# Kernel tuning notes

Measured on AMD Instinct MI355X. Metric: run time of the kernel, lower is better.

The kernel has to match this reference:

```python
import jax, jax.numpy as jnp
import numpy as np

D_MODEL = 1024
N_BLOCKS = 4
D_STATE = 16
D_CONV = 4
EXPAND = 2
DT_RANK = 64  # ceil(1024/16)
D_INNER = EXPAND * D_MODEL
BATCH = 2
SEQLEN = 1024


def setup_inputs() -> dict:
    key = jax.random.key(0)
    ks = jax.random.split(key, 8)
    s = 0.02
    f = lambda k, sh: (jax.random.normal(k, sh, dtype=jnp.float32) * s)
    return {
        "x": jax.random.normal(ks[0], (BATCH, SEQLEN, D_MODEL), dtype=jnp.float32),
        "norm_w": jnp.ones((N_BLOCKS, D_MODEL), jnp.float32),
        "norm_b": jnp.zeros((N_BLOCKS, D_MODEL), jnp.float32),
        "in_proj_w": f(ks[1], (N_BLOCKS, D_MODEL, 2 * D_INNER)),
        "conv_w": f(ks[2], (N_BLOCKS, D_INNER, D_CONV)),
        "conv_b": jnp.zeros((N_BLOCKS, D_INNER), jnp.float32),
        "xproj_w": f(ks[3], (N_BLOCKS, D_INNER, DT_RANK + 2 * D_STATE)),
        "dtproj_w": f(ks[4], (N_BLOCKS, DT_RANK, D_INNER)),
        "dtproj_b": jnp.full((N_BLOCKS, D_INNER), -4.6, jnp.float32),  # softplus ~ 0.01
        "A_log": jnp.tile(jnp.log(jnp.arange(1, D_STATE + 1, dtype=jnp.float32))[None, None, :], (N_BLOCKS, D_INNER, 1)),
        "skip_D": jnp.ones((N_BLOCKS, D_INNER), jnp.float32),
        "out_proj_w": f(ks[5], (N_BLOCKS, D_INNER, D_MODEL)),
        "fn_w": jnp.ones((D_MODEL,), jnp.float32),
        "fn_b": jnp.zeros((D_MODEL,), jnp.float32),
    }


def _layer_norm(x, w, b):
    m = jnp.mean(x, -1, keepdims=True)
    v = jnp.mean((x - m) ** 2, -1, keepdims=True)
    return (x - m) * jax.lax.rsqrt(v + 1e-5) * w + b


def _selective_scan(u, dt, A, Bm, Cm, Dp):
    # u, dt: (B,L,E)  A: (E,N)  Bm, Cm: (B,L,N)  Dp: (E,)
    dA = jnp.exp(dt[..., None] * A)                 # (B,L,E,N) ZOH discretization of A
    dBu = (dt * u)[..., None] * Bm[:, :, None, :]   # (B,L,E,N) Euler discretization of B*u

    def step(h, inp):
        dA_t, dBu_t, C_t = inp
        h = dA_t * h + dBu_t                        # (B,E,N)
        y = jnp.einsum('ben,bn->be', h, C_t)
        return h, y

    h0 = jnp.zeros((u.shape[0], u.shape[2], A.shape[1]), u.dtype)
    xs = (jnp.moveaxis(dA, 1, 0), jnp.moveaxis(dBu, 1, 0), jnp.moveaxis(Cm, 1, 0))
    _, ys = jax.lax.scan(step, h0, xs)
    y = jnp.moveaxis(ys, 0, 1)                      # (B,L,E)
    return y + u * Dp


def _mamba(x, in_w, cw, cb, xw, dtw, dtb, A_log, Dp, ow):
    L = x.shape[1]
    xz = x @ in_w                                   # (B,L,2E)
    u, z = jnp.split(xz, 2, axis=-1)
    K = cw.shape[1]
    up = jnp.pad(u, ((0, 0), (K - 1, 0), (0, 0)))   # causal depthwise conv
    conv = cb + sum(up[:, k:k + L, :] * cw[:, k] for k in range(K))
    u = jax.nn.silu(conv)
    dbl = u @ xw                                    # (B,L,R+2N)
    dt = jax.nn.softplus(dbl[..., :DT_RANK] @ dtw + dtb)
    Bm = dbl[..., DT_RANK:DT_RANK + D_STATE]
    Cm = dbl[..., DT_RANK + D_STATE:]
    A = -jnp.exp(A_log)
    y = _selective_scan(u, dt, A, Bm, Cm, Dp)
    y = y * jax.nn.silu(z)                          # gating branch
    return y @ ow


def _forward(x, norm_w, norm_b, in_proj_w, conv_w, conv_b, xproj_w, dtproj_w, dtproj_b, A_log, skip_D, out_proj_w, fn_w, fn_b):
    for i in range(N_BLOCKS):
        h = _layer_norm(x, norm_w[i], norm_b[i])
        h = _mamba(h, in_proj_w[i], conv_w[i], conv_b[i], xproj_w[i], dtproj_w[i], dtproj_b[i], A_log[i], skip_D[i], out_proj_w[i])
        x = x + h                                   # pre-norm residual
    return _layer_norm(x, fn_w, fn_b)


def reference(x, norm_w, norm_b, in_proj_w, conv_w, conv_b, xproj_w, dtproj_w, dtproj_b, A_log, skip_D, out_proj_w, fn_w, fn_b):
    return _forward(x, norm_w, norm_b, in_proj_w, conv_w, conv_b, xproj_w, dtproj_w, dtproj_b, A_log, skip_D, out_proj_w, fn_w, fn_b)
```

## Files before the change

kernel.cpp:

```cpp
#include <hip/hip_runtime.h>
#include <hip/hip_bf16.h>
#include <math.h>

#define BATCH 2
#define SEQLEN 1024
#define DMODEL 1024
#define DINNER 2048
#define DSTATE 16
#define DTRANK 64
#define XDIM 96
#define KCONV 4
#define NBLOCKS 4
#define MROWS (BATCH*SEQLEN)

#define NCHUNK 32
#define CLEN (SEQLEN/NCHUNK)
#define SUN 4

typedef short bf16x8 __attribute__((ext_vector_type(8)));
typedef unsigned short u16x8 __attribute__((ext_vector_type(8)));
typedef float f32x4 __attribute__((ext_vector_type(4)));

__device__ __forceinline__ unsigned short f2bf(float x) {
    union { float f; unsigned u; } c; c.f = x;
    unsigned r = c.u + 0x7FFFu + ((c.u >> 16) & 1u);
    return (unsigned short)(r >> 16);
}
__device__ __forceinline__ float bf2f(unsigned short h) {
    union { unsigned u; float f; } c; c.u = (unsigned)h << 16;
    return c.f;
}

__device__ __forceinline__ void gload16(const void* src, void* dst) {
    __builtin_amdgcn_global_load_lds(
        (const __attribute__((address_space(1))) void*)src,
        (__attribute__((address_space(3))) void*)dst, 16, 0, 0);
}

__global__ __launch_bounds__(256) void lnc_k(const float* __restrict__ x,
    const float* __restrict__ w, const float* __restrict__ b,
    float* __restrict__ resid, unsigned short* __restrict__ out)
{
    int row = blockIdx.x;
    int tid = threadIdx.x;
    size_t off = (size_t)row * DMODEL + tid * 4;
    float4 v = *(const float4*)(x + off);
    *(float4*)(resid + off) = v;
    float s  = v.x + v.y + v.z + v.w;
    float sq = v.x*v.x + v.y*v.y + v.z*v.z + v.w*v.w;
    #pragma unroll
    for (int o = 32; o > 0; o >>= 1) {
        s  += __shfl_down(s, o);
        sq += __shfl_down(sq, o);
    }
    __shared__ float ss[4], sq4[4];
    int wid = tid >> 6;
    if ((tid & 63) == 0) { ss[wid] = s; sq4[wid] = sq; }
    __syncthreads();
    if (tid == 0) {
        ss[0]  = ss[0] + ss[1] + ss[2] + ss[3];
        sq4[0] = sq4[0] + sq4[1] + sq4[2] + sq4[3];
    }
    __syncthreads();
    float mean = ss[0] * (1.0f / DMODEL);
    float var  = sq4[0] * (1.0f / DMODEL) - mean * mean;
    float rstd = rsqrtf(var + 1e-5f);
    float4 wv = *(const float4*)(w + tid * 4);
    float4 bv = *(const float4*)(b + tid * 4);
    ushort4 h;
    h.x = f2bf((v.x - mean) * rstd * wv.x + bv.x);
    h.y = f2bf((v.y - mean) * rstd * wv.y + bv.y);
    h.z = f2bf((v.z - mean) * rstd * wv.z + bv.z);
    h.w = f2bf((v.w - mean) * rstd * wv.w + bv.w);
    *(ushort4*)(out + off) = h;
}

template<int FINAL>
__global__ __launch_bounds__(256) void predln_k(
    const float* __restrict__ pout, float* __restrict__ resid,
    const float* __restrict__ w, const float* __restrict__ b,
    unsigned short* __restrict__ hb16, float* __restrict__ fout)
{
    int row = blockIdx.x;
    int tid = threadIdx.x;
    const size_t MN = (size_t)MROWS * DMODEL;
    size_t off = (size_t)row * DMODEL + tid * 4;
    float4 p0 = *(const float4*)(pout + off);
    float4 p1 = *(const float4*)(pout + off + MN);
    float4 p2 = *(const float4*)(pout + off + 2 * MN);
    float4 p3 = *(const float4*)(pout + off + 3 * MN);
    float4 r  = *(const float4*)(resid + off);
    float4 v;
    v.x = r.x + (p0.x + p1.x) + (p2.x + p3.x);
    v.y = r.y + (p0.y + p1.y) + (p2.y + p3.y);
    v.z = r.z + (p0.z + p1.z) + (p2.z + p3.z);
    v.w = r.w + (p0.w + p1.w) + (p2.w + p3.w);
    if (!FINAL) *(float4*)(resid + off) = v;

    float s  = v.x + v.y + v.z + v.w;
    float sq = v.x*v.x + v.y*v.y + v.z*v.z + v.w*v.w;
    #pragma unroll
    for (int o = 32; o > 0; o >>= 1) {
        s  += __shfl_down(s, o);
        sq += __shfl_down(sq, o);
    }
    __shared__ float ss[4], sq4[4];
    int wid = tid >> 6;
    if ((tid & 63) == 0) { ss[wid] = s; sq4[wid] = sq; }
    __syncthreads();
    if (tid == 0) {
        ss[0]  = ss[0] + ss[1] + ss[2] + ss[3];
        sq4[0] = sq4[0] + sq4[1] + sq4[2] + sq4[3];
    }
    __syncthreads();
    float mean = ss[0] * (1.0f / DMODEL);
    float var  = sq4[0] * (1.0f / DMODEL) - mean * mean;
    float rstd = rsqrtf(var + 1e-5f);
    float4 wv = *(const float4*)(w + tid * 4);
    float4 bv = *(const float4*)(b + tid * 4);
    float o0 = (v.x - mean) * rstd * wv.x + bv.x;
    float o1 = (v.y - mean) * rstd * wv.y + bv.y;
    float o2 = (v.z - mean) * rstd * wv.z + bv.z;
    float o3 = (v.w - mean) * rstd * wv.w + bv.w;
    if (FINAL) {
        *(float4*)(fout + off) = make_float4(o0, o1, o2, o3);
    } else {
        ushort4 h;
        h.x = f2bf(o0); h.y = f2bf(o1); h.z = f2bf(o2); h.w = f2bf(o3);
        *(ushort4*)(hb16 + off) = h;
    }
}

__global__ __launch_bounds__(256) void wtr2_k(
    const float* __restrict__ W, unsigned short* __restrict__ WT,
    int N, int K, long long wstride, long long wtstride)
{
    const float* Wl = W + (size_t)blockIdx.z * wstride;
    unsigned short* WTl = WT + (size_t)blockIdx.z * wtstride;
    __shared__ float T[64][65];
    int n0 = blockIdx.x * 64, k0 = blockIdx.y * 64;
    int tid = threadIdx.x;
    int kk = tid >> 4, nn = (tid & 15) * 4;
    #pragma unroll
    for (int p = 0; p < 4; ++p) {
        float4 v = make_float4(0.f, 0.f, 0.f, 0.f);
        if (n0 + nn + 4 <= N)
            v = *(const float4*)(Wl + (size_t)(k0 + p * 16 + kk) * N + n0 + nn);
        T[p * 16 + kk][nn + 0] = v.x;
        T[p * 16 + kk][nn + 1] = v.y;
        T[p * 16 + kk][nn + 2] = v.z;
        T[p * 16 + kk][nn + 3] = v.w;
    }
    __syncthreads();
    int n2 = tid >> 4, k2 = (tid & 15) * 4;
    #pragma unroll
    for (int p = 0; p < 4; ++p) {
        int nrow = n0 + p * 16 + n2;
        ushort4 h = {0, 0, 0, 0};
        if (nrow < N) {
            h.x = f2bf(T[k2 + 0][p * 16 + n2]);
            h.y = f2bf(T[k2 + 1][p * 16 + n2]);
            h.z = f2bf(T[k2 + 2][p * 16 + n2]);
            h.w = f2bf(T[k2 + 3][p * 16 + n2]);
        }
        *(ushort4*)(WTl + (size_t)nrow * K + k0 + k2) = h;
    }
}

template<int EPI, int BN, int SWZX = 0, int SWZY = 0>
__global__ __launch_bounds__(256) void mgemm6_k(
    const unsigned short* __restrict__ A,
    const unsigned short* __restrict__ BT,
    float* __restrict__ out0, float* __restrict__ out1,
    const float* __restrict__ bias,
    int N, int Kf, int Kloc)
{
    constexpr int WN = BN / 2;
    constexpr int NJ = WN / 16;
    __shared__ unsigned short As[3][128 * 32];
    __shared__ unsigned short Bs[3][BN * 32];
    int tid = threadIdx.x;
    int lane = tid & 63, w = tid >> 6;
    int wr = w >> 1, wc = w & 1;
    int bxx = blockIdx.x, byy = blockIdx.y;
    if constexpr (SWZX > 0) {
        constexpr int TOT = SWZX * SWZY;
        int f = bxx + SWZX * byy;
        int nf = (f & 7) * (TOT / 8) + (f >> 3);
        bxx = nf % SWZX; byy = nf / SWZX;
    }
    int m0 = byy * 128, n0 = bxx * BN;
    int lr = lane & 15, G = lane >> 4;

    int ra0 = w * 32 + (lane >> 2);
    int ra1 = ra0 + 16;
    int ga0 = (lane & 3) ^ ((ra0 >> 1) & 3);
    int ga1 = (lane & 3) ^ ((ra1 >> 1) & 3);
    int rb0 = w * (BN / 4) + (lane >> 2);
    int gb0 = (lane & 3) ^ ((rb0 >> 1) & 3);
    int rb1 = rb0 + 16;
    int gb1 = (lane & 3) ^ ((rb1 >> 1) & 3);

    int kz = blockIdx.z * Kloc;
    const unsigned short* pa0 = A  + (size_t)(m0 + ra0) * Kf + kz + ga0 * 8;
    const unsigned short* pa1 = A  + (size_t)(m0 + ra1) * Kf + kz + ga1 * 8;
    const unsigned short* pb0 = BT + (size_t)(n0 + rb0) * Kf + kz + gb0 * 8;
    const unsigned short* pb1 = BT + (size_t)(n0 + rb1) * Kf + kz + gb1 * 8;
    int dA0 = (w * 32) * 32, dA1 = dA0 + 16 * 32;
    int dB0 = (w * (BN / 4)) * 32, dB1 = dB0 + 16 * 32;

#define ISSUE(tt, bufi) do {                                   \
        gload16(pa0 + (tt) * 32, &As[bufi][dA0]);              \
        gload16(pa1 + (tt) * 32, &As[bufi][dA1]);              \
        gload16(pb0 + (tt) * 32, &Bs[bufi][dB0]);              \
        if (BN == 128) gload16(pb1 + (tt) * 32, &Bs[bufi][dB1]); \
    } while (0)

    f32x4 acc[4][NJ] = {};
    int T = Kloc / 32;

    ISSUE(0, 0);
    if (T > 1) ISSUE(1, 1);

    int cur = 0;
    for (int t = 0; t < T; ++t) {
        if (t + 1 < T) {
            if constexpr (BN == 128)
                asm volatile("s_waitcnt vmcnt(4)" ::: "memory");
            else
                asm volatile("s_waitcnt vmcnt(3)" ::: "memory");
        } else {
            asm volatile("s_waitcnt vmcnt(0)" ::: "memory");
        }
        __builtin_amdgcn_s_barrier();
        if (t + 2 < T) {
            int nb = cur + 2; if (nb >= 3) nb -= 3;
            ISSUE(t + 2, nb);
        }
        bf16x8 af[4], bfr[NJ];
        #pragma unroll
        for (int i = 0; i < 4; ++i) {
            int r = wr * 64 + i * 16 + lr;
            af[i] = *(const bf16x8*)&As[cur][r * 32 + ((G ^ ((r >> 1) & 3)) << 3)];
        }
        #pragma unroll
        for (int j = 0; j < NJ; ++j) {
            int r = wc * WN + j * 16 + lr;
            bfr[j] = *(const bf16x8*)&Bs[cur][r * 32 + ((G ^ ((r >> 1) & 3)) << 3)];
        }
        #pragma unroll
        for (int i = 0; i < 4; ++i)
            #pragma unroll
            for (int j = 0; j < NJ; ++j)
                acc[i][j] = __builtin_amdgcn_mfma_f32_16x16x32_bf16(
                    af[i], bfr[j], acc[i][j], 0, 0, 0);
        __builtin_amdgcn_s_barrier();
        cur = (cur + 1 == 3) ? 0 : cur + 1;
    }
#undef ISSUE

    int rbase = m0 + wr * 64 + (lane >> 4) * 4;
    int cbase = n0 + wc * WN + lr;
    #pragma unroll
    for (int i = 0; i < 4; ++i)
        #pragma unroll
        for (int j = 0; j < NJ; ++j)
            #pragma unroll
            for (int r = 0; r < 4; ++r) {
                int row = rbase + i * 16 + r;
                int col = cbase + j * 16;
                float c = acc[i][j][r];
                if (EPI == 0) {
                    if (col < DINNER)
                        ((unsigned short*)out0)[(size_t)row * DINNER + col] = f2bf(c);
                    else
                        ((unsigned short*)out1)[(size_t)row * DINNER + (col - DINNER)] = f2bf(c);
                } else if (EPI == 2) {
                    out0[(size_t)blockIdx.z * MROWS * N + (size_t)row * N + col] = c;
                } else if (EPI == 3) {
                    if (col < XDIM)
                        out0[(size_t)blockIdx.z * MROWS * XDIM +
                             (size_t)row * XDIM + col] = c;
                } else {
                    float cc = c + bias[col];
                    cc = fmaxf(cc, 0.f) + log1pf(__expf(-fabsf(cc)));
                    ((unsigned short*)out0)[(size_t)row * N + col] = f2bf(cc);
                }
            }
}

#define XSPLIT 16
__global__ __launch_bounds__(256) void xprojR_k(
    const float* __restrict__ part, float* __restrict__ dbl,
    unsigned short* __restrict__ db64)
{
    int idx = blockIdx.x * 256 + threadIdx.x;
    float s = 0.f;
    #pragma unroll
    for (int k = 0; k < XSPLIT; ++k)
        s += part[(size_t)k * MROWS * XDIM + idx];
    dbl[idx] = s;
    int col = idx % XDIM;
    if (col < DTRANK)
        db64[(size_t)(idx / XDIM) * DTRANK + col] = f2bf(s);
}

__global__ __launch_bounds__(256) void conv_k(const unsigned short* __restrict__ u,
    const float* __restrict__ cw, const float* __restrict__ cb,
    unsigned short* __restrict__ out)
{
    int idx = blockIdx.x * 256 + threadIdx.x;
    int c8 = idx & (DINNER / 8 - 1);
    int t  = (idx >> 8) & (SEQLEN - 1);
    int b  = idx >> 18;
    int e0 = c8 * 8;
    size_t base = (size_t)b * SEQLEN * DINNER + (size_t)t * DINNER + e0;
    u16x8 rows[KCONV];
    #pragma unroll
    for (int k = 0; k < KCONV; ++k) {
        int tt = t + k - (KCONV - 1);
        u16x8 zv = {0,0,0,0,0,0,0,0};
        rows[k] = (tt >= 0) ?
            *(const u16x8*)(u + base + (size_t)(k - (KCONV - 1)) * DINNER) : zv;
    }
    u16x8 o;
    #pragma unroll
    for (int j = 0; j < 8; ++j) {
        float4 wv = *(const float4*)(cw + (size_t)(e0 + j) * KCONV);
        float acc = cb[e0 + j];
        acc = fmaf(bf2f(rows[0][j]), wv.x, acc);
        acc = fmaf(bf2f(rows[1][j]), wv.y, acc);
        acc = fmaf(bf2f(rows[2][j]), wv.z, acc);
        acc = fmaf(bf2f(rows[3][j]), wv.w, acc);
        o[j] = f2bf(acc / (1.f + __expf(-acc)));
    }
    *(u16x8*)(out + base) = o;
}

template<int CTRL>
__device__ __forceinline__ float qadd(float x) {
    int y = __builtin_amdgcn_update_dpp(0, __float_as_int(x), CTRL, 0xF, 0xF, true);
    return x + __int_as_float(y);
}

__global__ __launch_bounds__(512) void scan_k(
    const unsigned short* __restrict__ dt, const unsigned short* __restrict__ uc,
    const float* __restrict__ dbl, const unsigned short* __restrict__ z,
    const float* __restrict__ A_log, const float* __restrict__ Dp,
    unsigned short* __restrict__ yout)
{
    __shared__ float sAlo[NCHUNK][8][2][4], sAhi[NCHUNK][8][2][4];
    __shared__ float sBlo[NCHUNK][8][2][4], sBhi[NCHUNK][8][2][4];
    int tid = threadIdx.x;
    int sub = tid & 1;
    int ei  = (tid >> 1) & 7;
    int ch  = tid >> 4;
    int bid = blockIdx.x;
    int blk = (bid & 7) * 64 + (bid >> 3);
    int eg  = blk & 255;
    int b   = blk >> 8;
    int e   = eg * 8 + ei;

    const float L2E = 1.4426950408889634f;
    float AstL2[8];
    {
        const float* ap = A_log + (size_t)e * DSTATE + sub * 8;
        #pragma unroll
        for (int q = 0; q < 2; ++q) {
            float4 v = *(const float4*)(ap + q * 4);
            AstL2[q * 4 + 0] = -__expf(v.x) * L2E;
            AstL2[q * 4 + 1] = -__expf(v.y) * L2E;
            AstL2[q * 4 + 2] = -__expf(v.z) * L2E;
            AstL2[q * 4 + 3] = -__expf(v.w) * L2E;
        }
    }
    size_t base_e = (size_t)b * SEQLEN * DINNER + e;
    size_t base_x = (size_t)b * SEQLEN * XDIM + DTRANK + sub * 8;
    int t0c = ch * CLEN;

    float h[8] = {0.f, 0.f, 0.f, 0.f, 0.f, 0.f, 0.f, 0.f};
    float ssum = 0.f;
    for (int t0 = t0c; t0 < t0c + CLEN; t0 += SUN) {
        float sdt[SUN], su[SUN];
        #pragma unroll
        for (int u = 0; u < SUN; ++u) {
            size_t te = base_e + (size_t)(t0 + u) * DINNER;
            sdt[u] = bf2f(dt[te]);
            su[u]  = bf2f(uc[te]);
        }
        #pragma unroll
        for (int u = 0; u < SUN; ++u) {
            const float* dx = dbl + base_x + (size_t)(t0 + u) * XDIM;
            float4 bn0 = *(const float4*)(dx);
            float4 bn1 = *(const float4*)(dx + 4);
            float dtu = sdt[u] * su[u];
            ssum += sdt[u];
            h[0] = fmaf(__builtin_amdgcn_exp2f(sdt[u] * AstL2[0]), h[0], dtu * bn0.x);
            h[1] = fmaf(__builtin_amdgcn_exp2f(sdt[u] * AstL2[1]), h[1], dtu * bn0.y);
            h[2] = fmaf(__builtin_amdgcn_exp2f(sdt[u] * AstL2[2]), h[2], dtu * bn0.z);
            h[3] = fmaf(__builtin_amdgcn_exp2f(sdt[u] * AstL2[3]), h[3], dtu * bn0.w);
            h[4] = fmaf(__builtin_amdgcn_exp2f(sdt[u] * AstL2[4]), h[4], dtu * bn1.x);
            h[5] = fmaf(__builtin_amdgcn_exp2f(sdt[u] * AstL2[5]), h[5], dtu * bn1.y);
            h[6] = fmaf(__builtin_amdgcn_exp2f(sdt[u] * AstL2[6]), h[6], dtu * bn1.z);
            h[7] = fmaf(__builtin_amdgcn_exp2f(sdt[u] * AstL2[7]), h[7], dtu * bn1.w);
        }
    }
    float a_[8];
    #pragma unroll
    for (int i = 0; i < 8; ++i) a_[i] = __builtin_amdgcn_exp2f(AstL2[i] * ssum);
    *(f32x4*)&sAlo[ch][ei][sub][0] = *(f32x4*)&a_[0];
    *(f32x4*)&sAhi[ch][ei][sub][0] = *(f32x4*)&a_[4];
    *(f32x4*)&sBlo[ch][ei][sub][0] = *(f32x4*)&h[0];
    *(f32x4*)&sBhi[ch][ei][sub][0] = *(f32x4*)&h[4];
    __syncthreads();

    #pragma unroll
    for (int s = 1; s < NCHUNK; s <<= 1) {
        float pa[8], pb[8];
        bool act = (ch >= s);
        if (act) {
            *(f32x4*)&pa[0] = *(const f32x4*)&sAlo[ch - s][ei][sub][0];
            *(f32x4*)&pa[4] = *(const f32x4*)&sAhi[ch - s][ei][sub][0];
            *(f32x4*)&pb[0] = *(const f32x4*)&sBlo[ch - s][ei][sub][0];
            *(f32x4*)&pb[4] = *(const f32x4*)&sBhi[ch - s][ei][sub][0];
        }
        __syncthreads();
        if (act) {
            #pragma unroll
            for (int i = 0; i < 8; ++i) {
                h[i]  = fmaf(a_[i], pb[i], h[i]);
                a_[i] *= pa[i];
            }
            *(f32x4*)&sAlo[ch][ei][sub][0] = *(f32x4*)&a_[0];
            *(f32x4*)&sAhi[ch][ei][sub][0] = *(f32x4*)&a_[4];
            *(f32x4*)&sBlo[ch][ei][sub][0] = *(f32x4*)&h[0];
            *(f32x4*)&sBhi[ch][ei][sub][0] = *(f32x4*)&h[4];
        }
        __syncthreads();
    }

    if (ch > 0) {
        *(f32x4*)&h[0] = *(const f32x4*)&sBlo[ch - 1][ei][sub][0];
        *(f32x4*)&h[4] = *(const f32x4*)&sBhi[ch - 1][ei][sub][0];
    } else {
        #pragma unroll
        for (int i = 0; i < 8; ++i) h[i] = 0.f;
    }

    float Dk = Dp[e];
    for (int t0 = t0c; t0 < t0c + CLEN; t0 += SUN) {
        float sdt[SUN], su[SUN], zz[SUN];
        #pragma unroll
        for (int u = 0; u < SUN; ++u) {
            size_t te = base_e + (size_t)(t0 + u) * DINNER;
            sdt[u] = bf2f(dt[te]);
            su[u]  = bf2f(uc[te]);
            zz[u]  = bf2f(z[te]);
        }
        #pragma unroll
        for (int u = 0; u < SUN; ++u) {
            const float* dx = dbl + base_x + (size_t)(t0 + u) * XDIM;
            float4 bn0 = *(const float4*)(dx);
            float4 bn1 = *(const float4*)(dx + 4);
            float4 cn0 = *(const float4*)(dx + 16);
            float4 cn1 = *(const float4*)(dx + 20);
            float dtu = sdt[u] * su[u];
            h[0] = fmaf(__builtin_amdgcn_exp2f(sdt[u] * AstL2[0]), h[0], dtu * bn0.x);
            h[1] = fmaf(__builtin_amdgcn_exp2f(sdt[u] * AstL2[1]), h[1], dtu * bn0.y);
            h[2] = fmaf(__builtin_amdgcn_exp2f(sdt[u] * AstL2[2]), h[2], dtu * bn0.z);
            h[3] = fmaf(__builtin_amdgcn_exp2f(sdt[u] * AstL2[3]), h[3], dtu * bn0.w);
            h[4] = fmaf(__builtin_amdgcn_exp2f(sdt[u] * AstL2[4]), h[4], dtu * bn1.x);
            h[5] = fmaf(__builtin_amdgcn_exp2f(sdt[u] * AstL2[5]), h[5], dtu * bn1.y);
            h[6] = fmaf(__builtin_amdgcn_exp2f(sdt[u] * AstL2[6]), h[6], dtu * bn1.z);
            h[7] = fmaf(__builtin_amdgcn_exp2f(sdt[u] * AstL2[7]), h[7], dtu * bn1.w);
            float p = h[0] * cn0.x + h[1] * cn0.y + h[2] * cn0.z + h[3] * cn0.w
                    + h[4] * cn1.x + h[5] * cn1.y + h[6] * cn1.z + h[7] * cn1.w;
            p = qadd<0xB1>(p);
            if (sub == 0) {
                float zvv = zz[u];
                float yv = p + su[u] * Dk;
                yout[base_e + (size_t)(t0 + u) * DINNER] =
                    f2bf(yv * (zvv / (1.f + __expf(-zvv))));
            }
        }
    }
}

extern "C" void kernel_launch(void* const* d_in, const int* in_sizes, int n_in,
                              void* d_out, int out_size, void* d_ws, size_t ws_size,
                              hipStream_t stream)
{
    const float* x         = (const float*)d_in[0];
    const float* norm_w    = (const float*)d_in[1];
    const float* norm_b    = (const float*)d_in[2];
    const float* in_proj_w = (const float*)d_in[3];
    const float* conv_w    = (const float*)d_in[4];
    const float* conv_b    = (const float*)d_in[5];
    const float* xproj_w   = (const float*)d_in[6];
    const float* dtproj_w  = (const float*)d_in[7];
    const float* dtproj_b  = (const float*)d_in[8];
    const float* A_log     = (const float*)d_in[9];
    const float* skip_D    = (const float*)d_in[10];
    const float* out_proj_w= (const float*)d_in[11];
    const float* fn_w      = (const float*)d_in[12];
    const float* fn_b      = (const float*)d_in[13];

    float* resid = (float*)d_out;
    float* ws    = (float*)d_ws;
    const size_t M1 = 1024 * 1024;
    unsigned short* wtib = (unsigned short*)(ws);
    unsigned short* wtob = (unsigned short*)(ws + 8  * M1);
    unsigned short* wtxp = (unsigned short*)(ws + 12 * M1);
    unsigned short* wtdt = (unsigned short*)(ws + 12 * M1 + M1 / 2);
    unsigned short* hb16 = (unsigned short*)(ws + 13 * M1);
    unsigned short* ub16 = (unsigned short*)(ws + 14 * M1);
    unsigned short* zb16 = (unsigned short*)(ws + 16 * M1);
    unsigned short* ucb16= (unsigned short*)(ws + 18 * M1);
    unsigned short* dtb16= (unsigned short*)(ws + 20 * M1);
    float*          dblb = ws + 22 * M1;
    unsigned short* db64 = (unsigned short*)(ws + 22 * M1 + M1 / 4);
    unsigned short* yb16 = (unsigned short*)(ws + 23 * M1);
    float*          xpart= ws + 25 * M1;
    float*          pout = ws + 28 * M1;

    wtr2_k<<<dim3(2 * DINNER / 64, DMODEL / 64, NBLOCKS), 256, 0, stream>>>(
        in_proj_w, wtib, 2 * DINNER, DMODEL,
        (long long)DMODEL * 2 * DINNER, (long long)2 * DINNER * DMODEL);
    wtr2_k<<<dim3(DMODEL / 64, DINNER / 64, NBLOCKS), 256, 0, stream>>>(
        out_proj_w, wtob, DMODEL, DINNER,
        (long long)DINNER * DMODEL, (long long)DMODEL * DINNER);
    wtr2_k<<<dim3(2, DINNER / 64, NBLOCKS), 256, 0, stream>>>(
        xproj_w, wtxp, XDIM, DINNER,
        (long long)DINNER * XDIM, (long long)128 * DINNER);
    wtr2_k<<<dim3(DINNER / 64, 1, NBLOCKS), 256, 0, stream>>>(
        dtproj_w, wtdt, DINNER, DTRANK,
        (long long)DTRANK * DINNER, (long long)DINNER * DTRANK);

    lnc_k<<<MROWS, 256, 0, stream>>>(x, norm_w, norm_b, resid, hb16);

    for (int i = 0; i < NBLOCKS; ++i) {
        mgemm6_k<0, 128, 32, 16><<<dim3(2 * DINNER / 128, MROWS / 128, 1), 256, 0, stream>>>(
            hb16, wtib + (size_t)i * 2 * DINNER * DMODEL,
            (float*)ub16, (float*)zb16, nullptr, 2 * DINNER, DMODEL, DMODEL);
        conv_k<<<(MROWS * DINNER / 8) / 256, 256, 0, stream>>>(
            ub16, conv_w + (size_t)i * DINNER * KCONV,
            conv_b + (size_t)i * DINNER, ucb16);
        mgemm6_k<3, 128><<<dim3(1, MROWS / 128, XSPLIT), 256, 0, stream>>>(
            ucb16, wtxp + (size_t)i * 128 * DINNER,
            xpart, nullptr, nullptr, XDIM, DINNER, DINNER / XSPLIT);
        xprojR_k<<<(MROWS * XDIM) / 256, 256, 0, stream>>>(xpart, dblb, db64);
        mgemm6_k<4, 64><<<dim3(DINNER / 64, MROWS / 128, 1), 256, 0, stream>>>(
            db64, wtdt + (size_t)i * DINNER * DTRANK,
            (float*)dtb16, nullptr, dtproj_b + (size_t)i * DINNER,
            DINNER, DTRANK, DTRANK);
        scan_k<<<BATCH * DINNER / 8, 512, 0, stream>>>(
            dtb16, ucb16, dblb, zb16,
            A_log + (size_t)i * DINNER * DSTATE, skip_D + (size_t)i * DINNER, yb16);
        mgemm6_k<2, 128, 8, 16><<<dim3(DMODEL / 128, MROWS / 128, 4), 256, 0, stream>>>(
            yb16, wtob + (size_t)i * DMODEL * DINNER,
            pout, nullptr, nullptr, DMODEL, DINNER, DINNER / 4);
        if (i < NBLOCKS - 1)
            predln_k<0><<<MROWS, 256, 0, stream>>>(pout, resid,
                norm_w + (i + 1) * DMODEL, norm_b + (i + 1) * DMODEL,
                hb16, nullptr);
        else
            predln_k<1><<<MROWS, 256, 0, stream>>>(pout, resid,
                fn_w, fn_b, nullptr, resid);
    }
}
```

Measured before the change: 571.0 us.

## Add 256x128-tile 512-thread GEMM kernel for in_proj and out_proj

Adds a new MFMA GEMM kernel with a larger 256x128 output tile, 8 waves per block, triple-buffered LDS and an XOR-swizzled layout. It replaces the 128-row tile kernel for the in_proj and out_proj GEMMs, keeping the block-index swizzle. The aim is more data reuse per block and fewer redundant global loads. The trade-off is more LDS per block (about 72KB) and fewer blocks in flight, which may lower occupancy.

Result: slower. 594.5 us (+4.1%).

```diff
diff --git a/kernel.cpp b/kernel.cpp
--- a/kernel.cpp
+++ b/kernel.cpp
@@ -270,12 +270,7 @@
                 int row = rbase + i * 16 + r;
                 int col = cbase + j * 16;
                 float c = acc[i][j][r];
-                if (EPI == 0) {
-                    if (col < DINNER)
-                        ((unsigned short*)out0)[(size_t)row * DINNER + col] = f2bf(c);
-                    else
-                        ((unsigned short*)out1)[(size_t)row * DINNER + (col - DINNER)] = f2bf(c);
-                } else if (EPI == 2) {
+                if (EPI == 2) {
                     out0[(size_t)blockIdx.z * MROWS * N + (size_t)row * N + col] = c;
                 } else if (EPI == 3) {
                     if (col < XDIM)
@@ -285,6 +280,109 @@
                     float cc = c + bias[col];
                     cc = fmaxf(cc, 0.f) + log1pf(__expf(-fabsf(cc)));
                     ((unsigned short*)out0)[(size_t)row * N + col] = f2bf(cc);
+                }
+            }
+}
+
+template<int EPI, int SWZX = 0, int SWZY = 0>
+__global__ __launch_bounds__(512) void mgemm8_k(
+    const unsigned short* __restrict__ A,
+    const unsigned short* __restrict__ BT,
+    float* __restrict__ out0, float* __restrict__ out1,
+    int N, int Kf, int Kloc)
+{
+    __shared__ unsigned short As[3][256 * 32];
+    __shared__ unsigned short Bs[3][128 * 32];
+    int tid = threadIdx.x;
+    int lane = tid & 63, w = tid >> 6;
+    int wr = w >> 1, wc = w & 1;
+    int bxx = blockIdx.x, byy = blockIdx.y;
+    if constexpr (SWZX > 0) {
+        constexpr int TOT = SWZX * SWZY;
+        int f = bxx + SWZX * byy;
+        int nf = (f & 7) * (TOT / 8) + (f >> 3);
+        bxx = nf % SWZX; byy = nf / SWZX;
+    }
+    int m0 = byy * 256, n0 = bxx * 128;
+    int lr = lane & 15, G = lane >> 4;
+
+    int ra0 = w * 32 + (lane >> 2);
+    int ra1 = ra0 + 16;
+    int ga0 = (lane & 3) ^ ((ra0 >> 1) & 3);
+    int ga1 = (lane & 3) ^ ((ra1 >> 1) & 3);
+    int rb0 = w * 16 + (lane >> 2);
+    int gb0 = (lane & 3) ^ ((rb0 >> 1) & 3);
+
+    int kz = blockIdx.z * Kloc;
+    const unsigned short* pa0 = A  + (size_t)(m0 + ra0) * Kf + kz + ga0 * 8;
+    const unsigned short* pa1 = A  + (size_t)(m0 + ra1) * Kf + kz + ga1 * 8;
+    const unsigned short* pb0 = BT + (size_t)(n0 + rb0) * Kf + kz + gb0 * 8;
+    int dA0 = (w * 32) * 32, dA1 = dA0 + 16 * 32;
+    int dB0 = (w * 16) * 32;
+
+#define ISSUE8(tt, bufi) do {                                  \
+        gload16(pa0 + (tt) * 32, &As[bufi][dA0]);              \
+        gload16(pa1 + (tt) * 32, &As[bufi][dA1]);              \
+        gload16(pb0 + (tt) * 32, &Bs[bufi][dB0]);              \
+    } while (0)
+
+    f32x4 acc[4][4] = {};
+    int T = Kloc / 32;
+
+    ISSUE8(0, 0);
+    if (T > 1) ISSUE8(1, 1);
+
+    int cur = 0;
+    for (int t = 0; t < T; ++t) {
+        if (t + 1 < T)
+            asm volatile("s_waitcnt vmcnt(3)" ::: "memory");
+        else
+            asm volatile("s_waitcnt vmcnt(0)" ::: "memory");
+        __builtin_amdgcn_s_barrier();
+        if (t + 2 < T) {
+            int nb = cur + 2; if (nb >= 3) nb -= 3;
+            ISSUE8(t + 2, nb);
+        }
+        bf16x8 af[4], bfr[4];
+        #pragma unroll
+        for (int i = 0; i < 4; ++i) {
+            int r = wr * 64 + i * 16 + lr;
+            af[i] = *(const bf16x8*)&As[cur][r * 32 + ((G ^ ((r >> 1) & 3)) << 3)];
+        }
+        #pragma unroll
+        for (int j = 0; j < 4; ++j) {
+            int r = wc * 64 + j * 16 + lr;
+            bfr[j] = *(const bf16x8*)&Bs[cur][r * 32 + ((G ^ ((r >> 1) & 3)) << 3)];
+        }
+        #pragma unroll
+        for (int i = 0; i < 4; ++i)
+            #pragma unroll
+            for (int j = 0; j < 4; ++j)
+                acc[i][j] = __builtin_amdgcn_mfma_f32_16x16x32_bf16(
+                    af[i], bfr[j], acc[i][j], 0, 0, 0);
+        __builtin_amdgcn_s_barrier();
+        cur = (cur + 1 == 3) ? 0 : cur + 1;
+    }
+#undef ISSUE8
+
+    int rbase = m0 + wr * 64 + (lane >> 4) * 4;
+    int cbase = n0 + wc * 64 + lr;
+    #pragma unroll
+    for (int i = 0; i < 4; ++i)
+        #pragma unroll
+        for (int j = 0; j < 4; ++j)
+            #pragma unroll
+            for (int r = 0; r < 4; ++r) {
+                int row = rbase + i * 16 + r;
+                int col = cbase + j * 16;
+                float c = acc[i][j][r];
+                if (EPI == 0) {
+                    if (col < DINNER)
+                        ((unsigned short*)out0)[(size_t)row * DINNER + col] = f2bf(c);
+                    else
+                        ((unsigned short*)out1)[(size_t)row * DINNER + (col - DINNER)] = f2bf(c);
+                } else {
+                    out0[(size_t)blockIdx.z * MROWS * N + (size_t)row * N + col] = c;
                 }
             }
 }
@@ -539,9 +637,9 @@
     lnc_k<<<MROWS, 256, 0, stream>>>(x, norm_w, norm_b, resid, hb16);
 
     for (int i = 0; i < NBLOCKS; ++i) {
-        mgemm6_k<0, 128, 32, 16><<<dim3(2 * DINNER / 128, MROWS / 128, 1), 256, 0, stream>>>(
+        mgemm8_k<0, 32, 8><<<dim3(2 * DINNER / 128, MROWS / 256, 1), 512, 0, stream>>>(
             hb16, wtib + (size_t)i * 2 * DINNER * DMODEL,
-            (float*)ub16, (float*)zb16, nullptr, 2 * DINNER, DMODEL, DMODEL);
+            (float*)ub16, (float*)zb16, 2 * DINNER, DMODEL, DMODEL);
         conv_k<<<(MROWS * DINNER / 8) / 256, 256, 0, stream>>>(
             ub16, conv_w + (size_t)i * DINNER * KCONV,
             conv_b + (size_t)i * DINNER, ucb16);
@@ -556,9 +654,9 @@
         scan_k<<<BATCH * DINNER / 8, 512, 0, stream>>>(
             dtb16, ucb16, dblb, zb16,
             A_log + (size_t)i * DINNER * DSTATE, skip_D + (size_t)i * DINNER, yb16);
-        mgemm6_k<2, 128, 8, 16><<<dim3(DMODEL / 128, MROWS / 128, 4), 256, 0, stream>>>(
+        mgemm8_k<2, 8, 8><<<dim3(DMODEL / 128, MROWS / 256, 4), 512, 0, stream>>>(
             yb16, wtob + (size_t)i * DMODEL * DINNER,
-            pout, nullptr, nullptr, DMODEL, DINNER, DINNER / 4);
+            pout, nullptr, DMODEL, DINNER, DINNER / 4);
         if (i < NBLOCKS - 1)
             predln_k<0><<<MROWS, 256, 0, stream>>>(pout, resid,
                 norm_w + (i + 1) * DMODEL, norm_b + (i + 1) * DMODEL,
```
